# Kernel optimization log

Measured on AMD Instinct MI355X. Metric: run time of the kernel, lower is better.

The kernel has to match this reference:

```python
import jax, jax.numpy as jnp
import numpy as np

B, T, D, H = 2, 2048, 1024, 16
HD = D // H  # head_dim = 64


def setup_inputs() -> dict:
    key = jax.random.key(0)
    ks = jax.random.split(key, 5)
    s = 0.02
    return {
        "x": jax.random.normal(ks[0], (B, T, D), dtype=jnp.float32),
        "Wqkv": jax.random.normal(ks[1], (3 * D, D), dtype=jnp.float32) * s,
        "bqkv": jax.random.normal(ks[2], (3 * D,), dtype=jnp.float32) * s,
        "Wproj": jax.random.normal(ks[3], (D, D), dtype=jnp.float32) * s,
        "bproj": jax.random.normal(ks[4], (D,), dtype=jnp.float32) * s,
    }


def reference(x, Wqkv, bqkv, Wproj, bproj):
    b, t, d = x.shape
    qkv = x @ Wqkv.T + bqkv                      # [B,T,3D]
    q, k, v = jnp.split(qkv, 3, axis=-1)
    # [B,T,D] -> [B,H,T,HD]
    def to_heads(u):
        return u.reshape(b, t, H, HD).transpose(0, 2, 1, 3)
    q, k, v = to_heads(q), to_heads(k), to_heads(v)
    scale = 1.0 / jnp.sqrt(jnp.float32(HD))
    attn = jnp.einsum("bhqd,bhkd->bhqk", q, k) * scale   # [B,H,T,T]
    causal = jnp.tril(jnp.ones((t, t), dtype=bool))
    attn = jnp.where(causal[None, None, :, :], attn, -jnp.inf)
    attn = jax.nn.softmax(attn, axis=-1)
    scores = jnp.einsum("bhqk,bhkd->bhqd", attn, v)       # [B,H,T,HD]
    scores = scores.transpose(0, 2, 1, 3).reshape(b, t, d)
    return scores @ Wproj.T + bproj
```

## Files before the change

### kernel.cpp

```cpp
#include <hip/hip_runtime.h>

typedef __bf16 bf16_8 __attribute__((ext_vector_type(8)));
typedef __bf16 bf16_4 __attribute__((ext_vector_type(4)));
typedef float  f32_4  __attribute__((ext_vector_type(4)));
typedef short  s16x4  __attribute__((ext_vector_type(4)));

typedef __attribute__((address_space(1))) const void* as1_cvp;
typedef __attribute__((address_space(3))) void*       as3_vp;

__device__ __forceinline__ void load16_to_lds(const void* g, void* l) {
    __builtin_amdgcn_global_load_lds((as1_cvp)g, (as3_vp)l, 16, 0, 0);
}

__device__ __forceinline__ f32_4 mfma16x16x16(bf16_4 a, bf16_4 b, f32_4 c) {
#if __has_builtin(__builtin_amdgcn_mfma_f32_16x16x16_bf16)
    return __builtin_amdgcn_mfma_f32_16x16x16_bf16(a, b, c, 0, 0, 0);
#else
    return __builtin_amdgcn_mfma_f32_16x16x16bf16_1k(
        __builtin_bit_cast(s16x4, a), __builtin_bit_cast(s16x4, b), c, 0, 0, 0);
#endif
}

__device__ __forceinline__ float fast_exp2(float x) {
#if __has_builtin(__builtin_amdgcn_exp2f)
    return __builtin_amdgcn_exp2f(x);
#else
    return exp2f(x);
#endif
}

__global__ __launch_bounds__(256) void cvt_all(
    const float* __restrict__ a, const float* __restrict__ b,
    const float* __restrict__ c, __bf16* __restrict__ out,
    int na4, int nb4, int nc4)
{
    int i = blockIdx.x * 256 + threadIdx.x;
    if (i >= na4 + nb4 + nc4) return;
    float4 f;
    if (i < na4)            f = ((const float4*)a)[i];
    else if (i < na4 + nb4) f = ((const float4*)b)[i - na4];
    else                    f = ((const float4*)c)[i - na4 - nb4];
    bf16_4 v = { (__bf16)f.x, (__bf16)f.y, (__bf16)f.z, (__bf16)f.w };
    ((bf16_4*)out)[i] = v;
}

#define BM 128

template<int OUT_BF16, int BN_, int QKV>
__global__ __launch_bounds__(256) void gemm_bt(
    const __bf16* __restrict__ A,
    const __bf16* __restrict__ B,
    const float*  __restrict__ bias,
    __bf16* __restrict__ Cb, float* __restrict__ Cf,
    __bf16* __restrict__ Vtb,
    int M, int N, int K, int ldc)
{
    constexpr int NT   = BN_ / 32;
    constexpr int CSTR = BN_ + (OUT_BF16 ? 8 : 4);
    __shared__ __align__(16) char smem[35840];
    __bf16* As = (__bf16*)smem;
    __bf16* Bs = As + 128 * 64;

    const int tid  = threadIdx.x;
    const int wave = tid >> 6;
    const int lane = tid & 63;
    const int wm = wave >> 1, wn = wave & 1;
    const int quad = lane >> 4, l16 = lane & 15;
    const int bm = blockIdx.y * BM, bn = blockIdx.x * BN_;

    const int r0 = tid >> 3;
    const int ch = tid & 7;
    const int cs = (ch ^ (r0 & 7)) * 8;

    f32_4 acc[4][NT];
    #pragma unroll
    for (int i = 0; i < 4; ++i)
        #pragma unroll
        for (int j = 0; j < NT; ++j)
            acc[i][j] = f32_4{0.f, 0.f, 0.f, 0.f};

    for (int k0 = 0; k0 < K; k0 += 64) {
        __syncthreads();
        #pragma unroll
        for (int p = 0; p < 4; ++p) {
            int row = p * 32 + r0;
            load16_to_lds(A + (size_t)(bm + row) * K + k0 + cs,
                          &As[(p * 32 + wave * 8) * 64]);
        }
        #pragma unroll
        for (int p = 0; p < BN_ / 32; ++p) {
            int row = p * 32 + r0;
            load16_to_lds(B + (size_t)(bn + row) * K + k0 + cs,
                          &Bs[(p * 32 + wave * 8) * 64]);
        }
        __syncthreads();

        #pragma unroll
        for (int h = 0; h < 2; ++h) {
            const int sl = ((quad + h * 4) ^ (l16 & 7)) * 8;
            bf16_8 af[4], bfr[NT];
            #pragma unroll
            for (int mt = 0; mt < 4; ++mt)
                af[mt] = *(const bf16_8*)&As[(wm * 64 + mt * 16 + l16) * 64 + sl];
            #pragma unroll
            for (int nt = 0; nt < NT; ++nt)
                bfr[nt] = *(const bf16_8*)&Bs[(wn * (BN_/2) + nt * 16 + l16) * 64 + sl];
            #pragma unroll
            for (int mt = 0; mt < 4; ++mt)
                #pragma unroll
                for (int nt = 0; nt < NT; ++nt)
                    acc[mt][nt] = __builtin_amdgcn_mfma_f32_16x16x32_bf16(
                        af[mt], bfr[nt], acc[mt][nt], 0, 0, 0);
        }
    }

    if (QKV && bn >= 2048) {
        const int b_ = bm >> 11;
        const int t0 = (bm & 2047) + wm * 64;
        #pragma unroll
        for (int nt = 0; nt < NT; ++nt) {
            int vrow = (bn - 2048) + wn * (BN_/2) + nt * 16 + l16;
            float bv = bias ? bias[2048 + vrow] : 0.f;
            #pragma unroll
            for (int mt = 0; mt < 4; ++mt) {
                bf16_4 ov;
                #pragma unroll
                for (int r = 0; r < 4; ++r)
                    ov[r] = (__bf16)(acc[mt][nt][r] + bv);
                *(bf16_4*)(Vtb + ((size_t)b_ * 1024 + vrow) * 2048
                           + t0 + mt * 16 + quad * 4) = ov;
            }
        }
        return;
    }

    __syncthreads();

    if (OUT_BF16) {
        __bf16* Cs = (__bf16*)smem;
        #pragma unroll
        for (int mt = 0; mt < 4; ++mt)
            #pragma unroll
            for (int nt = 0; nt < NT; ++nt) {
                int col = wn * (BN_/2) + nt * 16 + l16;
                float bv = bias ? bias[bn + col] : 0.f;
                #pragma unroll
                for (int r = 0; r < 4; ++r)
                    Cs[(wm * 64 + mt * 16 + quad * 4 + r) * CSTR + col] =
                        (__bf16)(acc[mt][nt][r] + bv);
            }
        __syncthreads();
        const int rr = tid >> 4, cc = (tid & 15) * 8;
        #pragma unroll
        for (int p = 0; p < 8; ++p) {
            int row = p * 16 + rr;
            bf16_8 v = *(const bf16_8*)&Cs[row * CSTR + cc];
            *(bf16_8*)(Cb + (size_t)(bm + row) * ldc + bn + cc) = v;
        }
    } else {
        float* Cs = (float*)smem;
        #pragma unroll
        for (int mt = 0; mt < 4; ++mt)
            #pragma unroll
            for (int nt = 0; nt < NT; ++nt) {
                int col = wn * (BN_/2) + nt * 16 + l16;
                float bv = bias ? bias[bn + col] : 0.f;
                #pragma unroll
                for (int r = 0; r < 4; ++r)
                    Cs[(wm * 64 + mt * 16 + quad * 4 + r) * CSTR + col] =
                        acc[mt][nt][r] + bv;
            }
        __syncthreads();
        const int rr = tid >> 4, cc = (tid & 15) * 4;
        #pragma unroll
        for (int p = 0; p < 8; ++p) {
            int row = p * 16 + rr;
            float4 v = *(const float4*)&Cs[row * CSTR + cc];
            *(float4*)(Cf + (size_t)(bm + row) * ldc + bn + cc) = v;
        }
    }
}

__global__ __launch_bounds__(512, 4) void attn_kernel(
    const __bf16* __restrict__ qk, const __bf16* __restrict__ vt,
    __bf16* __restrict__ out)
{
    constexpr int T = 2048;
    __shared__ __align__(16) char pool[35328];
    __bf16* Ks = (__bf16*)pool;
    __bf16* Vt = (__bf16*)(pool + 16384);
    float*  Om = (float*)pool;
    float*  Lm = (float*)(pool + 34816);

    const int tid  = threadIdx.x;
    const int wave = tid >> 6;
    const int lane = tid & 63;
    const int wg = wave >> 2, wq = wave & 3;
    const int quad = lane >> 4, l16 = lane & 15;

    const int fid  = blockIdx.x;
    const int xcd  = fid & 7;
    const int half = fid >> 8;
    const int w    = (fid >> 3) & 31;
    const int qt   = half ? (7 - (w >> 2)) : ((w >> 2) + 8);
    const int bh   = xcd * 4 + (w & 3);
    const int b = bh >> 4, h = bh & 15;
    const int jmax = 2 * qt + 1;

    const size_t rowbase = (size_t)b * T;
    const __bf16* Kbase = qk + 1024 + h * 64;
    const __bf16* Vbase = vt + (size_t)bh * 64 * 2048;

    const int srow = tid >> 3;
    const int sch  = tid & 7;
    const int schf = sch ^ (srow & 7);

    constexpr float QSCALE = 0.125f * 1.4426950408889634f;
    bf16_8 aq[2][2];
    #pragma unroll
    for (int mt = 0; mt < 2; ++mt) {
        const __bf16* qrow =
            qk + (rowbase + qt * 128 + wq * 32 + mt * 16 + l16) * 2048 + h * 64;
        aq[mt][0] = *(const bf16_8*)(qrow + quad * 8);
        aq[mt][1] = *(const bf16_8*)(qrow + 32 + quad * 8);
        #pragma unroll
        for (int u = 0; u < 8; ++u) {
            aq[mt][0][u] = (__bf16)((float)aq[mt][0][u] * QSCALE);
            aq[mt][1][u] = (__bf16)((float)aq[mt][1][u] * QSCALE);
        }
    }

    load16_to_lds(Kbase + (rowbase + srow) * 2048 + schf * 8, &Ks[wave * 512]);
    load16_to_lds(Vbase + (size_t)srow * 2048 + schf * 8,     &Vt[wave * 512]);

    float l_i[2] = {0.f, 0.f};
    f32_4 O[2][4];
    #pragma unroll
    for (int mt = 0; mt < 2; ++mt)
        #pragma unroll
        for (int dt = 0; dt < 4; ++dt) O[mt][dt] = f32_4{0.f, 0.f, 0.f, 0.f};

    for (int j = 0; j <= jmax; ++j) {
        const int cur = j & 1, nxt = cur ^ 1;
        __syncthreads();

        if (j < jmax) {
            const int jn = j + 1;
            load16_to_lds(Kbase + (rowbase + jn * 64 + srow) * 2048 + schf * 8,
                          &Ks[nxt * 4096 + wave * 512]);
            load16_to_lds(Vbase + (size_t)srow * 2048 + jn * 64 + schf * 8,
                          &Vt[nxt * 4096 + wave * 512]);
        }

        f32_4 S[2][2];
        __builtin_amdgcn_s_setprio(1);
        #pragma unroll
        for (int nt = 0; nt < 2; ++nt) {
            int rk = wg * 32 + nt * 16 + l16;
            int rx = rk & 7;
            bf16_8 kb0 = *(const bf16_8*)&Ks[cur * 4096 + rk * 64 + ((quad ^ rx) << 3)];
            bf16_8 kb1 = *(const bf16_8*)&Ks[cur * 4096 + rk * 64 + (((quad + 4) ^ rx) << 3)];
            #pragma unroll
            for (int mt = 0; mt < 2; ++mt) {
                f32_4 zz = {0.f, 0.f, 0.f, 0.f};
                zz = __builtin_amdgcn_mfma_f32_16x16x32_bf16(kb0, aq[mt][0], zz, 0, 0, 0);
                zz = __builtin_amdgcn_mfma_f32_16x16x32_bf16(kb1, aq[mt][1], zz, 0, 0, 0);
                S[mt][nt] = zz;
            }
        }
        __builtin_amdgcn_s_setprio(0);

        const bool diag = (j >= 2 * qt);
        bf16_4 bp[2][2];
        #pragma unroll
        for (int mt = 0; mt < 2; ++mt) {
            int qg = qt * 128 + wq * 32 + mt * 16 + l16;
            #pragma unroll
            for (int nt = 0; nt < 2; ++nt) {
                #pragma unroll
                for (int rr = 0; rr < 4; ++rr) {
                    float p = fast_exp2(S[mt][nt][rr]);
                    if (diag) {
                        int key = j * 64 + wg * 32 + nt * 16 + quad * 4 + rr;
                        if (key > qg) p = 0.f;
                    }
                    l_i[mt] += p;
                    bp[mt][nt][rr] = (__bf16)p;
                }
            }
        }

        __builtin_amdgcn_s_setprio(1);
        #pragma unroll
        for (int dt = 0; dt < 4; ++dt) {
            int d = dt * 16 + l16;
            int dsw = d & 7;
            #pragma unroll
            for (int nt = 0; nt < 2; ++nt) {
                int chv = (wg * 4 + nt * 2 + (quad >> 1)) ^ dsw;
                bf16_4 vaf = *(const bf16_4*)&Vt[cur * 4096 + d * 64 + chv * 8 + (quad & 1) * 4];
                #pragma unroll
                for (int mt = 0; mt < 2; ++mt)
                    O[mt][dt] = mfma16x16x16(vaf, bp[mt][nt], O[mt][dt]);
            }
        }
        __builtin_amdgcn_s_setprio(0);
    }

    float lw[2];
    #pragma unroll
    for (int mt = 0; mt < 2; ++mt) {
        float v = l_i[mt];
        v += __shfl_xor(v, 16, 64);
        v += __shfl_xor(v, 32, 64);
        lw[mt] = v;
    }
    __syncthreads();
    if (wg == 1) {
        #pragma unroll
        for (int mt = 0; mt < 2; ++mt) {
            #pragma unroll
            for (int dt = 0; dt < 4; ++dt)
                *(f32_4*)&Om[(wq * 32 + mt * 16 + l16) * 68 + dt * 16 + quad * 4] = O[mt][dt];
            if (quad == 0) Lm[wq * 32 + mt * 16 + l16] = lw[mt];
        }
    }
    __syncthreads();
    if (wg == 0) {
        #pragma unroll
        for (int mt = 0; mt < 2; ++mt) {
            float inv = 1.f / (lw[mt] + Lm[wq * 32 + mt * 16 + l16]);
            int q = qt * 128 + wq * 32 + mt * 16 + l16;
            #pragma unroll
            for (int dt = 0; dt < 4; ++dt) {
                f32_4 o2 = *(const f32_4*)&Om[(wq * 32 + mt * 16 + l16) * 68 + dt * 16 + quad * 4];
                bf16_4 ov;
                #pragma unroll
                for (int rr = 0; rr < 4; ++rr)
                    ov[rr] = (__bf16)((O[mt][dt][rr] + o2[rr]) * inv);
                *(bf16_4*)(out + (rowbase + q) * 1024 + h * 64 + dt * 16 + quad * 4) = ov;
            }
        }
    }
}

extern "C" void kernel_launch(void* const* d_in, const int* in_sizes, int n_in,
                              void* d_out, int out_size, void* d_ws, size_t ws_size,
                              hipStream_t stream)
{
    constexpr int Bc = 2, Tc = 2048, Dc = 1024;
    constexpr int M  = Bc * Tc;
    constexpr int N1 = 3 * Dc;

    const float* x     = (const float*)d_in[0];
    const float* Wqkv  = (const float*)d_in[1];
    const float* bqkv  = (const float*)d_in[2];
    const float* Wproj = (const float*)d_in[3];
    const float* bproj = (const float*)d_in[4];
    float* outp = (float*)d_out;

    __bf16* xb     = (__bf16*)d_ws;
    __bf16* wqkvb  = xb     + (size_t)M * Dc;
    __bf16* wprojb = wqkvb  + (size_t)N1 * Dc;
    __bf16* qkb    = wprojb + (size_t)Dc * Dc;
    __bf16* vtb    = qkb    + (size_t)M * 2048;
    __bf16* attnb  = vtb    + (size_t)Bc * 1024 * 2048;

    {
        int na4 = M * Dc / 4, nb4 = N1 * Dc / 4, nc4 = Dc * Dc / 4;
        int n4 = na4 + nb4 + nc4;
        cvt_all<<<(n4 + 255) / 256, 256, 0, stream>>>(x, Wqkv, Wproj, xb, na4, nb4, nc4);
    }

    gemm_bt<1, 128, 1><<<dim3(N1 / 128, M / BM), 256, 0, stream>>>(
        xb, wqkvb, bqkv, qkb, nullptr, vtb, M, N1, Dc, 2048);

    attn_kernel<<<dim3(512), 512, 0, stream>>>(qkb, vtb, attnb);

    gemm_bt<0, 64, 0><<<dim3(Dc / 64, M / BM), 256, 0, stream>>>(
        attnb, wprojb, bproj, nullptr, outp, nullptr, M, Dc, Dc, Dc);
}
```

Measured before the change: 171.3 us.

## Split attention key tile across four wave groups with 64 query rows per wave

Reorganizes the 8 waves from 2 key-groups × 4 query-groups to 4 key-groups × 2 query-groups. Each wave now handles 64 query rows against 16 keys, so one K fragment and one V fragment load feed four MFMAs each, which cuts LDS reads per MFMA. The cost is twice the O accumulator registers per wave, which may pressure occupancy at launch bounds (512,4). The final reduction also grows from one to three serialized LDS accumulation stages.

```diff
diff --git a/kernel.cpp b/kernel.cpp
--- a/kernel.cpp
+++ b/kernel.cpp
@@ -195,7 +195,7 @@
     const int tid  = threadIdx.x;
     const int wave = tid >> 6;
     const int lane = tid & 63;
-    const int wg = wave >> 2, wq = wave & 3;
+    const int wg = wave >> 1, wq = wave & 1;
     const int quad = lane >> 4, l16 = lane & 15;
 
     const int fid  = blockIdx.x;
@@ -216,11 +216,11 @@
     const int schf = sch ^ (srow & 7);
 
     constexpr float QSCALE = 0.125f * 1.4426950408889634f;
-    bf16_8 aq[2][2];
+    bf16_8 aq[4][2];
     #pragma unroll
-    for (int mt = 0; mt < 2; ++mt) {
+    for (int mt = 0; mt < 4; ++mt) {
         const __bf16* qrow =
-            qk + (rowbase + qt * 128 + wq * 32 + mt * 16 + l16) * 2048 + h * 64;
+            qk + (rowbase + qt * 128 + wq * 64 + mt * 16 + l16) * 2048 + h * 64;
         aq[mt][0] = *(const bf16_8*)(qrow + quad * 8);
         aq[mt][1] = *(const bf16_8*)(qrow + 32 + quad * 8);
         #pragma unroll
@@ -233,10 +233,10 @@
     load16_to_lds(Kbase + (rowbase + srow) * 2048 + schf * 8, &Ks[wave * 512]);
     load16_to_lds(Vbase + (size_t)srow * 2048 + schf * 8,     &Vt[wave * 512]);
 
-    float l_i[2] = {0.f, 0.f};
-    f32_4 O[2][4];
+    float l_i[4] = {0.f, 0.f, 0.f, 0.f};
+    f32_4 O[4][4];
     #pragma unroll
-    for (int mt = 0; mt < 2; ++mt)
+    for (int mt = 0; mt < 4; ++mt)
         #pragma unroll
         for (int dt = 0; dt < 4; ++dt) O[mt][dt] = f32_4{0.f, 0.f, 0.f, 0.f};
 
@@ -252,41 +252,37 @@
                           &Vt[nxt * 4096 + wave * 512]);
         }
 
-        f32_4 S[2][2];
+        const int rk = wg * 16 + l16;
+        const int rx = rk & 7;
+        f32_4 S[4];
         __builtin_amdgcn_s_setprio(1);
-        #pragma unroll
-        for (int nt = 0; nt < 2; ++nt) {
-            int rk = wg * 32 + nt * 16 + l16;
-            int rx = rk & 7;
+        {
             bf16_8 kb0 = *(const bf16_8*)&Ks[cur * 4096 + rk * 64 + ((quad ^ rx) << 3)];
             bf16_8 kb1 = *(const bf16_8*)&Ks[cur * 4096 + rk * 64 + (((quad + 4) ^ rx) << 3)];
             #pragma unroll
-            for (int mt = 0; mt < 2; ++mt) {
+            for (int mt = 0; mt < 4; ++mt) {
                 f32_4 zz = {0.f, 0.f, 0.f, 0.f};
                 zz = __builtin_amdgcn_mfma_f32_16x16x32_bf16(kb0, aq[mt][0], zz, 0, 0, 0);
                 zz = __builtin_amdgcn_mfma_f32_16x16x32_bf16(kb1, aq[mt][1], zz, 0, 0, 0);
-                S[mt][nt] = zz;
+                S[mt] = zz;
             }
         }
         __builtin_amdgcn_s_setprio(0);
 
         const bool diag = (j >= 2 * qt);
-        bf16_4 bp[2][2];
-        #pragma unroll
-        for (int mt = 0; mt < 2; ++mt) {
-            int qg = qt * 128 + wq * 32 + mt * 16 + l16;
-            #pragma unroll
-            for (int nt = 0; nt < 2; ++nt) {
-                #pragma unroll
-                for (int rr = 0; rr < 4; ++rr) {
-                    float p = fast_exp2(S[mt][nt][rr]);
-                    if (diag) {
-                        int key = j * 64 + wg * 32 + nt * 16 + quad * 4 + rr;
-                        if (key > qg) p = 0.f;
-                    }
-                    l_i[mt] += p;
-                    bp[mt][nt][rr] = (__bf16)p;
+        bf16_4 bp[4];
+        #pragma unroll
+        for (int mt = 0; mt < 4; ++mt) {
+            int qg = qt * 128 + wq * 64 + mt * 16 + l16;
+            #pragma unroll
+            for (int rr = 0; rr < 4; ++rr) {
+                float p = fast_exp2(S[mt][rr]);
+                if (diag) {
+                    int key = j * 64 + wg * 16 + quad * 4 + rr;
+                    if (key > qg) p = 0.f;
                 }
+                l_i[mt] += p;
+                bp[mt][rr] = (__bf16)p;
             }
         }
 
@@ -295,45 +291,75 @@
         for (int dt = 0; dt < 4; ++dt) {
             int d = dt * 16 + l16;
             int dsw = d & 7;
-            #pragma unroll
-            for (int nt = 0; nt < 2; ++nt) {
-                int chv = (wg * 4 + nt * 2 + (quad >> 1)) ^ dsw;
-                bf16_4 vaf = *(const bf16_4*)&Vt[cur * 4096 + d * 64 + chv * 8 + (quad & 1) * 4];
-                #pragma unroll
-                for (int mt = 0; mt < 2; ++mt)
-                    O[mt][dt] = mfma16x16x16(vaf, bp[mt][nt], O[mt][dt]);
-            }
+            int chv = (wg * 2 + (quad >> 1)) ^ dsw;
+            bf16_4 vaf = *(const bf16_4*)&Vt[cur * 4096 + d * 64 + chv * 8 + (quad & 1) * 4];
+            #pragma unroll
+            for (int mt = 0; mt < 4; ++mt)
+                O[mt][dt] = mfma16x16x16(vaf, bp[mt], O[mt][dt]);
         }
         __builtin_amdgcn_s_setprio(0);
     }
 
-    float lw[2];
+    float lw[4];
     #pragma unroll
-    for (int mt = 0; mt < 2; ++mt) {
+    for (int mt = 0; mt < 4; ++mt) {
         float v = l_i[mt];
         v += __shfl_xor(v, 16, 64);
         v += __shfl_xor(v, 32, 64);
         lw[mt] = v;
     }
+
+    __syncthreads();
+    if (wg == 3) {
+        #pragma unroll
+        for (int mt = 0; mt < 4; ++mt) {
+            int row = wq * 64 + mt * 16 + l16;
+            #pragma unroll
+            for (int dt = 0; dt < 4; ++dt)
+                *(f32_4*)&Om[row * 68 + dt * 16 + quad * 4] = O[mt][dt];
+            if (quad == 0) Lm[row] = lw[mt];
+        }
+    }
+    __syncthreads();
+    if (wg == 2) {
+        #pragma unroll
+        for (int mt = 0; mt < 4; ++mt) {
+            int row = wq * 64 + mt * 16 + l16;
+            #pragma unroll
+            for (int dt = 0; dt < 4; ++dt) {
+                f32_4 o2 = *(const f32_4*)&Om[row * 68 + dt * 16 + quad * 4];
+                #pragma unroll
+                for (int rr = 0; rr < 4; ++rr) o2[rr] += O[mt][dt][rr];
+                *(f32_4*)&Om[row * 68 + dt * 16 + quad * 4] = o2;
+            }
+            if (quad == 0) Lm[row] += lw[mt];
+        }
+    }
     __syncthreads();
     if (wg == 1) {
         #pragma unroll
-        for (int mt = 0; mt < 2; ++mt) {
-            #pragma unroll
-            for (int dt = 0; dt < 4; ++dt)
-                *(f32_4*)&Om[(wq * 32 + mt * 16 + l16) * 68 + dt * 16 + quad * 4] = O[mt][dt];
-            if (quad == 0) Lm[wq * 32 + mt * 16 + l16] = lw[mt];
+        for (int mt = 0; mt < 4; ++mt) {
+            int row = wq * 64 + mt * 16 + l16;
+            #pragma unroll
+            for (int dt = 0; dt < 4; ++dt) {
+                f32_4 o2 = *(const f32_4*)&Om[row * 68 + dt * 16 + quad * 4];
+                #pragma unroll
+                for (int rr = 0; rr < 4; ++rr) o2[rr] += O[mt][dt][rr];
+                *(f32_4*)&Om[row * 68 + dt * 16 + quad * 4] = o2;
+            }
+            if (quad == 0) Lm[row] += lw[mt];
         }
     }
     __syncthreads();
     if (wg == 0) {
         #pragma unroll
-        for (int mt = 0; mt < 2; ++mt) {
-            float inv = 1.f / (lw[mt] + Lm[wq * 32 + mt * 16 + l16]);
-            int q = qt * 128 + wq * 32 + mt * 16 + l16;
+        for (int mt = 0; mt < 4; ++mt) {
+            int row = wq * 64 + mt * 16 + l16;
+            float inv = 1.f / (lw[mt] + Lm[row]);
+            int q = qt * 128 + row;
             #pragma unroll
             for (int dt = 0; dt < 4; ++dt) {
-                f32_4 o2 = *(const f32_4*)&Om[(wq * 32 + mt * 16 + l16) * 68 + dt * 16 + quad * 4];
+                f32_4 o2 = *(const f32_4*)&Om[row * 68 + dt * 16 + quad * 4];
                 bf16_4 ov;
                 #pragma unroll
                 for (int rr = 0; rr < 4; ++rr)
```

New measurement: 212.6 us. +24.1%, slower.

## Switch attention to 32x32x16 MFMA tiles with permlane-swapped P fragments and 4 waves

Applied to the files above, without the earlier changes.

Rewrites the attention inner loop to use 32x32x16 bf16 MFMA for both QK^T and PV, with each wave now owning 64 query rows. The block shrinks from 8 to 4 waves, so each thread loads two K/V rows per tile. P values are packed to bf16 pairs and rearranged across lane halves with v_permlane32_swap so they can feed the second MFMA directly from registers. This cuts LDS fragment reads and MFMA instruction count per FLOP, at the cost of more accumulator registers per wave and fewer waves per block.

```diff
diff --git a/kernel.cpp b/kernel.cpp
--- a/kernel.cpp
+++ b/kernel.cpp
@@ -2,23 +2,15 @@
 
 typedef __bf16 bf16_8 __attribute__((ext_vector_type(8)));
 typedef __bf16 bf16_4 __attribute__((ext_vector_type(4)));
+typedef __bf16 bf16_2 __attribute__((ext_vector_type(2)));
 typedef float  f32_4  __attribute__((ext_vector_type(4)));
-typedef short  s16x4  __attribute__((ext_vector_type(4)));
+typedef float  f32_16 __attribute__((ext_vector_type(16)));
 
 typedef __attribute__((address_space(1))) const void* as1_cvp;
 typedef __attribute__((address_space(3))) void*       as3_vp;
 
 __device__ __forceinline__ void load16_to_lds(const void* g, void* l) {
     __builtin_amdgcn_global_load_lds((as1_cvp)g, (as3_vp)l, 16, 0, 0);
-}
-
-__device__ __forceinline__ f32_4 mfma16x16x16(bf16_4 a, bf16_4 b, f32_4 c) {
-#if __has_builtin(__builtin_amdgcn_mfma_f32_16x16x16_bf16)
-    return __builtin_amdgcn_mfma_f32_16x16x16_bf16(a, b, c, 0, 0, 0);
-#else
-    return __builtin_amdgcn_mfma_f32_16x16x16bf16_1k(
-        __builtin_bit_cast(s16x4, a), __builtin_bit_cast(s16x4, b), c, 0, 0, 0);
-#endif
 }
 
 __device__ __forceinline__ float fast_exp2(float x) {
@@ -27,6 +19,16 @@
 #else
     return exp2f(x);
 #endif
+}
+
+__device__ __forceinline__ unsigned pk2(float lo, float hi) {
+    union { bf16_2 h; unsigned u; } t;
+    t.h = bf16_2{(__bf16)lo, (__bf16)hi};
+    return t.u;
+}
+
+__device__ __forceinline__ void pswap(unsigned &a, unsigned &b) {
+    asm("v_permlane32_swap_b32 %0, %1" : "+v"(a), "+v"(b));
 }
 
 __global__ __launch_bounds__(256) void cvt_all(
@@ -181,7 +183,7 @@
     }
 }
 
-__global__ __launch_bounds__(512, 4) void attn_kernel(
+__global__ __launch_bounds__(256, 2) void attn_kernel(
     const __bf16* __restrict__ qk, const __bf16* __restrict__ vt,
     __bf16* __restrict__ out)
 {
@@ -195,14 +197,14 @@
     const int tid  = threadIdx.x;
     const int wave = tid >> 6;
     const int lane = tid & 63;
-    const int wg = wave >> 2, wq = wave & 3;
-    const int quad = lane >> 4, l16 = lane & 15;
+    const int wq = wave & 1, wg = wave >> 1;
+    const int l32 = lane & 31, hh = lane >> 5;
 
     const int fid  = blockIdx.x;
     const int xcd  = fid & 7;
-    const int half = fid >> 8;
+    const int hsel = fid >> 8;
     const int w    = (fid >> 3) & 31;
-    const int qt   = half ? (7 - (w >> 2)) : ((w >> 2) + 8);
+    const int qt   = hsel ? (7 - (w >> 2)) : ((w >> 2) + 8);
     const int bh   = xcd * 4 + (w & 3);
     const int b = bh >> 4, h = bh & 15;
     const int jmax = 2 * qt + 1;
@@ -211,34 +213,39 @@
     const __bf16* Kbase = qk + 1024 + h * 64;
     const __bf16* Vbase = vt + (size_t)bh * 64 * 2048;
 
-    const int srow = tid >> 3;
-    const int sch  = tid & 7;
-    const int schf = sch ^ (srow & 7);
+    const int sr   = tid >> 3;
+    const int schf = (tid & 7) ^ (sr & 7);
 
     constexpr float QSCALE = 0.125f * 1.4426950408889634f;
-    bf16_8 aq[2][2];
+    bf16_8 aq[2][4];
     #pragma unroll
-    for (int mt = 0; mt < 2; ++mt) {
-        const __bf16* qrow =
-            qk + (rowbase + qt * 128 + wq * 32 + mt * 16 + l16) * 2048 + h * 64;
-        aq[mt][0] = *(const bf16_8*)(qrow + quad * 8);
-        aq[mt][1] = *(const bf16_8*)(qrow + 32 + quad * 8);
-        #pragma unroll
-        for (int u = 0; u < 8; ++u) {
-            aq[mt][0][u] = (__bf16)((float)aq[mt][0][u] * QSCALE);
-            aq[mt][1][u] = (__bf16)((float)aq[mt][1][u] * QSCALE);
-        }
-    }
-
-    load16_to_lds(Kbase + (rowbase + srow) * 2048 + schf * 8, &Ks[wave * 512]);
-    load16_to_lds(Vbase + (size_t)srow * 2048 + schf * 8,     &Vt[wave * 512]);
-
+    for (int qq = 0; qq < 2; ++qq)
+        #pragma unroll
+        for (int df = 0; df < 4; ++df) {
+            const __bf16* qp = qk + (rowbase + qt*128 + wq*64 + qq*32 + l32)*2048
+                               + h*64 + df*16 + hh*8;
+            bf16_8 v = *(const bf16_8*)qp;
+            #pragma unroll
+            for (int u = 0; u < 8; ++u) v[u] = (__bf16)((float)v[u] * QSCALE);
+            aq[qq][df] = v;
+        }
+
+    #pragma unroll
+    for (int p = 0; p < 2; ++p) {
+        load16_to_lds(Kbase + (rowbase + sr + 32*p)*2048 + schf*8,
+                      Ks + p*2048 + wave*512);
+        load16_to_lds(Vbase + (size_t)(sr + 32*p)*2048 + schf*8,
+                      Vt + p*2048 + wave*512);
+    }
+
+    f32_16 O[2][2];
+    #pragma unroll
+    for (int dt = 0; dt < 2; ++dt)
+        #pragma unroll
+        for (int qq = 0; qq < 2; ++qq)
+            #pragma unroll
+            for (int r = 0; r < 16; ++r) O[dt][qq][r] = 0.f;
     float l_i[2] = {0.f, 0.f};
-    f32_4 O[2][4];
-    #pragma unroll
-    for (int mt = 0; mt < 2; ++mt)
-        #pragma unroll
-        for (int dt = 0; dt < 4; ++dt) O[mt][dt] = f32_4{0.f, 0.f, 0.f, 0.f};
 
     for (int j = 0; j <= jmax; ++j) {
         const int cur = j & 1, nxt = cur ^ 1;
@@ -246,62 +253,76 @@
 
         if (j < jmax) {
             const int jn = j + 1;
-            load16_to_lds(Kbase + (rowbase + jn * 64 + srow) * 2048 + schf * 8,
-                          &Ks[nxt * 4096 + wave * 512]);
-            load16_to_lds(Vbase + (size_t)srow * 2048 + jn * 64 + schf * 8,
-                          &Vt[nxt * 4096 + wave * 512]);
-        }
-
-        f32_4 S[2][2];
+            #pragma unroll
+            for (int p = 0; p < 2; ++p) {
+                load16_to_lds(Kbase + (rowbase + jn*64 + sr + 32*p)*2048 + schf*8,
+                              Ks + nxt*4096 + p*2048 + wave*512);
+                load16_to_lds(Vbase + (size_t)(sr + 32*p)*2048 + jn*64 + schf*8,
+                              Vt + nxt*4096 + p*2048 + wave*512);
+            }
+        }
+
+        const int krow = wg*32 + l32;
+        const int ksw  = krow & 7;
+        f32_16 S[2];
         __builtin_amdgcn_s_setprio(1);
-        #pragma unroll
-        for (int nt = 0; nt < 2; ++nt) {
-            int rk = wg * 32 + nt * 16 + l16;
-            int rx = rk & 7;
-            bf16_8 kb0 = *(const bf16_8*)&Ks[cur * 4096 + rk * 64 + ((quad ^ rx) << 3)];
-            bf16_8 kb1 = *(const bf16_8*)&Ks[cur * 4096 + rk * 64 + (((quad + 4) ^ rx) << 3)];
-            #pragma unroll
-            for (int mt = 0; mt < 2; ++mt) {
-                f32_4 zz = {0.f, 0.f, 0.f, 0.f};
-                zz = __builtin_amdgcn_mfma_f32_16x16x32_bf16(kb0, aq[mt][0], zz, 0, 0, 0);
-                zz = __builtin_amdgcn_mfma_f32_16x16x32_bf16(kb1, aq[mt][1], zz, 0, 0, 0);
-                S[mt][nt] = zz;
-            }
+        bf16_8 kf[4];
+        #pragma unroll
+        for (int df = 0; df < 4; ++df)
+            kf[df] = *(const bf16_8*)&Ks[cur*4096 + krow*64 + (((2*df + hh) ^ ksw) << 3)];
+        #pragma unroll
+        for (int qq = 0; qq < 2; ++qq) {
+            f32_16 z;
+            #pragma unroll
+            for (int r = 0; r < 16; ++r) z[r] = 0.f;
+            #pragma unroll
+            for (int df = 0; df < 4; ++df)
+                z = __builtin_amdgcn_mfma_f32_32x32x16_bf16(kf[df], aq[qq][df], z, 0, 0, 0);
+            S[qq] = z;
         }
         __builtin_amdgcn_s_setprio(0);
 
-        const bool diag = (j >= 2 * qt);
-        bf16_4 bp[2][2];
-        #pragma unroll
-        for (int mt = 0; mt < 2; ++mt) {
-            int qg = qt * 128 + wq * 32 + mt * 16 + l16;
-            #pragma unroll
-            for (int nt = 0; nt < 2; ++nt) {
-                #pragma unroll
-                for (int rr = 0; rr < 4; ++rr) {
-                    float p = fast_exp2(S[mt][nt][rr]);
-                    if (diag) {
-                        int key = j * 64 + wg * 32 + nt * 16 + quad * 4 + rr;
-                        if (key > qg) p = 0.f;
-                    }
-                    l_i[mt] += p;
-                    bp[mt][nt][rr] = (__bf16)p;
+        const bool diag = (j >= 2*qt);
+        unsigned fr[2][8];
+        #pragma unroll
+        for (int qq = 0; qq < 2; ++qq) {
+            float pe[16];
+            const int qg = qt*128 + wq*64 + qq*32 + l32;
+            #pragma unroll
+            for (int r = 0; r < 16; ++r) {
+                float e = fast_exp2(S[qq][r]);
+                if (diag) {
+                    int key = j*64 + wg*32 + (r&3) + 8*(r>>2) + 4*hh;
+                    if (key > qg) e = 0.f;
                 }
-            }
+                pe[r] = e;
+                l_i[qq] += e;
+            }
+            unsigned A = pk2(pe[0],  pe[1]),  Bv = pk2(pe[2],  pe[3]),
+                     C = pk2(pe[4],  pe[5]),  D  = pk2(pe[6],  pe[7]),
+                     E = pk2(pe[8],  pe[9]),  F  = pk2(pe[10], pe[11]),
+                     G = pk2(pe[12], pe[13]), H  = pk2(pe[14], pe[15]);
+            pswap(A, C); pswap(Bv, D); pswap(E, G); pswap(F, H);
+            fr[qq][0] = A; fr[qq][1] = Bv; fr[qq][2] = C; fr[qq][3] = D;
+            fr[qq][4] = E; fr[qq][5] = F;  fr[qq][6] = G; fr[qq][7] = H;
         }
 
         __builtin_amdgcn_s_setprio(1);
         #pragma unroll
-        for (int dt = 0; dt < 4; ++dt) {
-            int d = dt * 16 + l16;
-            int dsw = d & 7;
-            #pragma unroll
-            for (int nt = 0; nt < 2; ++nt) {
-                int chv = (wg * 4 + nt * 2 + (quad >> 1)) ^ dsw;
-                bf16_4 vaf = *(const bf16_4*)&Vt[cur * 4096 + d * 64 + chv * 8 + (quad & 1) * 4];
-                #pragma unroll
-                for (int mt = 0; mt < 2; ++mt)
-                    O[mt][dt] = mfma16x16x16(vaf, bp[mt][nt], O[mt][dt]);
+        for (int kh = 0; kh < 2; ++kh) {
+            #pragma unroll
+            for (int dt = 0; dt < 2; ++dt) {
+                const int d = dt*32 + l32;
+                bf16_8 vf = *(const bf16_8*)&Vt[cur*4096 + d*64 +
+                                (((wg*4 + kh*2 + hh) ^ (d & 7)) << 3)];
+                #pragma unroll
+                for (int qq = 0; qq < 2; ++qq) {
+                    union { unsigned dw[4]; bf16_8 v; } u;
+                    u.dw[0] = fr[qq][kh*4+0]; u.dw[1] = fr[qq][kh*4+1];
+                    u.dw[2] = fr[qq][kh*4+2]; u.dw[3] = fr[qq][kh*4+3];
+                    O[dt][qq] = __builtin_amdgcn_mfma_f32_32x32x16_bf16(
+                        vf, u.v, O[dt][qq], 0, 0, 0);
+                }
             }
         }
         __builtin_amdgcn_s_setprio(0);
@@ -309,37 +330,46 @@
 
     float lw[2];
     #pragma unroll
-    for (int mt = 0; mt < 2; ++mt) {
-        float v = l_i[mt];
-        v += __shfl_xor(v, 16, 64);
+    for (int qq = 0; qq < 2; ++qq) {
+        float v = l_i[qq];
         v += __shfl_xor(v, 32, 64);
-        lw[mt] = v;
-    }
+        lw[qq] = v;
+    }
+
     __syncthreads();
     if (wg == 1) {
         #pragma unroll
-        for (int mt = 0; mt < 2; ++mt) {
-            #pragma unroll
-            for (int dt = 0; dt < 4; ++dt)
-                *(f32_4*)&Om[(wq * 32 + mt * 16 + l16) * 68 + dt * 16 + quad * 4] = O[mt][dt];
-            if (quad == 0) Lm[wq * 32 + mt * 16 + l16] = lw[mt];
+        for (int qq = 0; qq < 2; ++qq) {
+            const int qrow = wq*64 + qq*32 + l32;
+            #pragma unroll
+            for (int dt = 0; dt < 2; ++dt)
+                #pragma unroll
+                for (int g = 0; g < 4; ++g) {
+                    f32_4 t = { O[dt][qq][g*4+0], O[dt][qq][g*4+1],
+                                O[dt][qq][g*4+2], O[dt][qq][g*4+3] };
+                    *(f32_4*)&Om[qrow*68 + dt*32 + g*8 + hh*4] = t;
+                }
+            if (hh == 0) Lm[qrow] = lw[qq];
         }
     }
     __syncthreads();
     if (wg == 0) {
         #pragma unroll
-        for (int mt = 0; mt < 2; ++mt) {
-            float inv = 1.f / (lw[mt] + Lm[wq * 32 + mt * 16 + l16]);
-            int q = qt * 128 + wq * 32 + mt * 16 + l16;
-            #pragma unroll
-            for (int dt = 0; dt < 4; ++dt) {
-                f32_4 o2 = *(const f32_4*)&Om[(wq * 32 + mt * 16 + l16) * 68 + dt * 16 + quad * 4];
-                bf16_4 ov;
-                #pragma unroll
-                for (int rr = 0; rr < 4; ++rr)
-                    ov[rr] = (__bf16)((O[mt][dt][rr] + o2[rr]) * inv);
-                *(bf16_4*)(out + (rowbase + q) * 1024 + h * 64 + dt * 16 + quad * 4) = ov;
-            }
+        for (int qq = 0; qq < 2; ++qq) {
+            const int qrow = wq*64 + qq*32 + l32;
+            const float inv = 1.f / (lw[qq] + Lm[qrow]);
+            const size_t obase = (rowbase + qt*128 + qrow) * 1024 + h*64;
+            #pragma unroll
+            for (int dt = 0; dt < 2; ++dt)
+                #pragma unroll
+                for (int g = 0; g < 4; ++g) {
+                    f32_4 o2 = *(const f32_4*)&Om[qrow*68 + dt*32 + g*8 + hh*4];
+                    bf16_4 ov;
+                    #pragma unroll
+                    for (int r = 0; r < 4; ++r)
+                        ov[r] = (__bf16)((O[dt][qq][g*4+r] + o2[r]) * inv);
+                    *(bf16_4*)(out + obase + dt*32 + g*8 + hh*4) = ov;
+                }
         }
     }
 }
@@ -375,7 +405,7 @@
     gemm_bt<1, 128, 1><<<dim3(N1 / 128, M / BM), 256, 0, stream>>>(
         xb, wqkvb, bqkv, qkb, nullptr, vtb, M, N1, Dc, 2048);
 
-    attn_kernel<<<dim3(512), 512, 0, stream>>>(qkb, vtb, attnb);
+    attn_kernel<<<dim3(512), 256, 0, stream>>>(qkb, vtb, attnb);
 
     gemm_bt<0, 64, 0><<<dim3(Dc / 64, M / BM), 256, 0, stream>>>(
         attnb, wprojb, bproj, nullptr, outp, nullptr, M, Dc, Dc, Dc);
```

Result: slower. 176.1 us (+2.8%).
